# Performance work log

Hardware: AMD Instinct MI355X
Metric: run time of the kernel (lower is better)

## Reference

```python
import jax, jax.numpy as jnp
import numpy as np

MODES = 12

def _conv3x3_circular(x, w, b):
    # x: [B,C,H,W], w: [O,I,3,3] -> circular padding of 1 then VALID conv
    xp = jnp.pad(x, ((0, 0), (0, 0), (1, 1), (1, 1)), mode='wrap')
    y = jax.lax.conv_general_dilated(xp, w, window_strides=(1, 1), padding='VALID',
                                     dimension_numbers=('NCHW', 'OIHW', 'NCHW'))
    return y + b[None, :, None, None]

def _spectral_conv(x, w1, w2):
    # x: [B,C,H,W] real; w1, w2: [C,O,m1,m2] complex
    B, C, H, W = x.shape
    x_ft = jnp.fft.rfft2(x)  # [B,C,H,W//2+1] complex
    m1 = min(MODES, H // 2)
    m2 = min(MODES, W // 2 + 1)
    top = jnp.einsum('bixy,ioxy->boxy', x_ft[:, :, :m1, :m2], w1[:, :, :m1, :m2])
    bot = jnp.einsum('bixy,ioxy->boxy', x_ft[:, :, -m1:, :m2], w2[:, :, :m1, :m2])
    out_ft = jnp.zeros((B, w1.shape[1], H, W // 2 + 1), dtype=x_ft.dtype)
    out_ft = out_ft.at[:, :, :m1, :m2].set(top).at[:, :, -m1:, :m2].set(bot)
    return jnp.fft.irfft2(out_ft, s=(H, W))

def setup_inputs() -> dict:
    key = jax.random.key(0)
    ks = jax.random.split(key, 16)
    width = 32
    scale = 1.0 / (width * width)
    return {
        'x': jax.random.normal(ks[0], (64, 2, 128, 128), dtype=jnp.float32),
        'p_w': jax.random.normal(ks[1], (width, 2, 3, 3), dtype=jnp.float32) * 0.2,
        'p_b': jax.random.normal(ks[2], (width,), dtype=jnp.float32) * 0.1,
        'scw1r': jax.random.uniform(ks[3], (4, width, width, MODES, MODES), dtype=jnp.float32) * scale,
        'scw1i': jax.random.uniform(ks[4], (4, width, width, MODES, MODES), dtype=jnp.float32) * scale,
        'scw2r': jax.random.uniform(ks[5], (4, width, width, MODES, MODES), dtype=jnp.float32) * scale,
        'scw2i': jax.random.uniform(ks[6], (4, width, width, MODES, MODES), dtype=jnp.float32) * scale,
        'ww': jax.random.normal(ks[7], (4, width, width), dtype=jnp.float32) * (1.0 / np.sqrt(width)),
        'wb': jax.random.normal(ks[8], (4, width), dtype=jnp.float32) * 0.1,
        'q1_w': jax.random.normal(ks[9], (128, width), dtype=jnp.float32) * (1.0 / np.sqrt(width)),
        'q1_b': jax.random.normal(ks[10], (128,), dtype=jnp.float32) * 0.1,
        'q2_w': jax.random.normal(ks[11], (1, 128), dtype=jnp.float32) * (1.0 / np.sqrt(128.0)),
        'q2_b': jax.random.normal(ks[12], (1,), dtype=jnp.float32) * 0.1,
    }

def reference(x, p_w, p_b, scw1r, scw1i, scw2r, scw2i, ww, wb, q1_w, q1_b, q2_w, q2_b):
    h = _conv3x3_circular(x, p_w, p_b)  # lifting: [B,2,H,W] -> [B,width,H,W]
    for i in range(4):
        w1 = scw1r[i] + 1j * scw1i[i]
        w2 = scw2r[i] + 1j * scw2i[i]
        x1 = _spectral_conv(h, w1, w2)
        x2 = jnp.einsum('bihw,oi->bohw', h, ww[i]) + wb[i][None, :, None, None]
        h = jax.nn.gelu(x1 + x2, approximate=False)
    g = h.mean(axis=(2, 3))  # [B,width]
    g = jax.nn.gelu(g @ q1_w.T + q1_b, approximate=False)
    g = g @ q2_w.T + q2_b
    return jax.nn.sigmoid(g)
```

## Files before the change

### kernel.cpp

```cpp
#include <hip/hip_runtime.h>
#include <math.h>

#define B 64
#define CIN 2
#define CH 32
#define H 128
#define W 128
#define MODES 12
#define KY 24
#define KX 12
#define HW (H*W)
#define NMODE (KY*KX)

typedef float f32x2 __attribute__((ext_vector_type(2)));
__device__ __forceinline__ f32x2 mk2(float a, float b) { f32x2 r; r.x = a; r.y = b; return r; }

__device__ __forceinline__ float gelu_f(float x) {
    float ax = fabsf(x) * 0.70710678118654752f;
    float t  = __builtin_amdgcn_rcpf(1.0f + 0.3275911f * ax);
    float p  = t * (0.254829592f + t * (-0.284496736f + t * (1.421413741f +
               t * (-1.453152027f + t * 1.061405429f))));
    float e  = __expf(-ax * ax);
    float er = copysignf(1.0f - p * e, x);
    return 0.5f * x * (1.0f + er);
}

__global__ __launch_bounds__(256) void k_init_tables(
        float* cWkw, float* sWkw, float* cnsWwk,
        float* cnsH2, float* mnsH2) {
    int t = blockIdx.x * 256 + threadIdx.x;
    const float TWO_PI_OVER = 6.283185307179586476925f / 128.0f;
    if (t < MODES * W) {
        int k = t / W, w = t % W;
        int m = (k * w) & 127;
        float s, c;
        sincosf(TWO_PI_OVER * (float)m, &s, &c);
        cWkw[k * W + w] = c;  sWkw[k * W + w] = s;
        cnsWwk[(w * MODES + k) * 2]     = c;
        cnsWwk[(w * MODES + k) * 2 + 1] = -s;
    } else if (t < MODES * W + KY * H) {
        int u = t - MODES * W;
        int kyI = u / H, hh = u % H;
        int ky = (kyI < MODES) ? kyI : (H - MODES + (kyI - MODES));
        int m = (ky * hh) & 127;
        float s, c;
        sincosf(TWO_PI_OVER * (float)m, &s, &c);
        cnsH2[(hh * KY + kyI) * 2]     = c;
        cnsH2[(hh * KY + kyI) * 2 + 1] = s;
        mnsH2[(hh * KY + kyI) * 2]     = -s;
        mnsH2[(hh * KY + kyI) * 2 + 1] = c;
    }
}

__global__ __launch_bounds__(256) void k_reorder_w(
        const float* __restrict__ w1r, const float* __restrict__ w1i,
        const float* __restrict__ w2r, const float* __restrict__ w2i,
        float* __restrict__ wR) {
    int idx = blockIdx.x * 256 + threadIdx.x;
    if (idx >= 4 * NMODE * CH * CH) return;
    int o = idx & 31;
    int i = (idx >> 5) & 31;
    int m = (idx >> 10) % NMODE;
    int layer = idx / (NMODE * CH * CH);
    int kyI = m / KX, kx = m % KX;
    const float *sr, *si;
    int row;
    if (kyI < MODES) { sr = w1r; si = w1i; row = kyI; }
    else             { sr = w2r; si = w2i; row = kyI - MODES; }
    int src = ((layer * CH + i) * CH + o) * (MODES * MODES) + row * MODES + kx;
    wR[(size_t)idx * 2]     = sr[src];
    wR[(size_t)idx * 2 + 1] = si[src];
}

__global__ __launch_bounds__(256) void k_transpose_ww(
        const float* __restrict__ ww, float* __restrict__ wwT) {
    int idx = blockIdx.x * 256 + threadIdx.x;
    if (idx >= 4 * CH * CH) return;
    int l = idx / (CH * CH);
    int r = idx % (CH * CH);
    int i = r / CH, o = r % CH;
    wwT[idx] = ww[l * CH * CH + o * CH + i];
}

__global__ __launch_bounds__(128) void k_lift(
        const float* __restrict__ x, const float* __restrict__ pw,
        const float* __restrict__ pb, float* __restrict__ h) {
    int bh = blockIdx.x;
    int b = bh >> 7, hr = bh & 127;
    int w = threadIdx.x;
    int wl = (w + W - 1) & (W - 1), wr2 = (w + 1) & (W - 1);
    float xv[CIN][3][3];
    #pragma unroll
    for (int ic = 0; ic < CIN; ++ic) {
        const float* xc = x + (size_t)(b * CIN + ic) * HW;
        #pragma unroll
        for (int r = 0; r < 3; ++r) {
            int hh = (hr + r - 1 + H) & (H - 1);
            const float* xr = xc + hh * W;
            xv[ic][r][0] = xr[wl];
            xv[ic][r][1] = xr[w];
            xv[ic][r][2] = xr[wr2];
        }
    }
    for (int o = 0; o < CH; ++o) {
        float acc = pb[o];
        const float* wo = pw + o * CIN * 9;
        #pragma unroll
        for (int ic = 0; ic < CIN; ++ic)
            #pragma unroll
            for (int r = 0; r < 3; ++r)
                #pragma unroll
                for (int c3 = 0; c3 < 3; ++c3)
                    acc += xv[ic][r][c3] * wo[ic * 9 + r * 3 + c3];
        h[(size_t)(b * CH + o) * HW + hr * W + w] = acc;
    }
}

__global__ __launch_bounds__(256, 4) void k_dft_w(
        const float* __restrict__ h, const float* __restrict__ cnsWwk,
        float* __restrict__ Xw) {
    int row = blockIdx.x * 256 + threadIdx.x;
    const float* src = h + (size_t)row * W;
    f32x2 acc2[MODES];
    #pragma unroll
    for (int k = 0; k < MODES; ++k) acc2[k] = mk2(0.f, 0.f);
    for (int w4 = 0; w4 < W; w4 += 4) {
        float4 v = *(const float4*)(src + w4);
        #pragma unroll
        for (int j = 0; j < 4; ++j) {
            float xval = (j == 0) ? v.x : (j == 1) ? v.y : (j == 2) ? v.z : v.w;
            const f32x2* cns = (const f32x2*)(cnsWwk + (w4 + j) * MODES * 2);
            f32x2 xv2 = mk2(xval, xval);
            #pragma unroll
            for (int k = 0; k < MODES; ++k)
                acc2[k] += xv2 * cns[k];
        }
    }
    float2* dst = (float2*)(Xw + (size_t)row * MODES * 2);
    #pragma unroll
    for (int k = 0; k < MODES; ++k) dst[k] = make_float2(acc2[k].x, acc2[k].y);
}

__global__ __launch_bounds__(320) void k_dft_h(
        const float* __restrict__ Xw, const float* __restrict__ cnsH2,
        float* __restrict__ Xf) {
    __shared__ float4 xs4[H * KX / 2];
    const float2* xs = (const float2*)xs4;
    int bc = blockIdx.x;
    int tid = threadIdx.x;
    const float4* src = (const float4*)(Xw + (size_t)bc * H * KX * 2);
    #pragma unroll
    for (int r = 0; r < 3; ++r) {
        int idx = r * 320 + tid;
        if (idx < H * KX / 2) xs4[idx] = src[idx];
    }
    __syncthreads();
    if (tid < KY * KX) {
        int ky = tid / KX, kx = tid % KX;
        const float2* cs = (const float2*)cnsH2 + ky;
        float ar = 0.f, ai = 0.f;
        #pragma unroll 4
        for (int hh = 0; hh < H; ++hh) {
            float2 v = xs[hh * KX + kx];
            float2 t = cs[hh * KY];
            ar += v.x * t.x + v.y * t.y;
            ai += v.y * t.x - v.x * t.y;
        }
        ((float2*)Xf)[(size_t)tid * (B * CH) + bc] = make_float2(ar, ai);
    }
}

__global__ __launch_bounds__(256) void k_specmul(
        const float* __restrict__ Xf, const float* __restrict__ wRl,
        float* __restrict__ Yt) {
    int m = blockIdx.x;
    int o = threadIdx.x & 31;
    int bq = threadIdx.x >> 5;
    const f32x2* X  = (const f32x2*)Xf  + (size_t)m * (B * CH);
    const f32x2* Wm = (const f32x2*)wRl + (size_t)m * (CH * CH);
    f32x2 acc2[8];
    #pragma unroll
    for (int j = 0; j < 8; ++j) acc2[j] = mk2(0.f, 0.f);
    for (int i = 0; i < CH; ++i) {
        f32x2 wv  = Wm[i * CH + o];
        f32x2 wvB = mk2(-wv.y, wv.x);
        #pragma unroll
        for (int j = 0; j < 8; ++j) {
            f32x2 xv = X[(bq * 8 + j) * CH + i];
            acc2[j] += mk2(xv.x, xv.x) * wv + mk2(xv.y, xv.y) * wvB;
        }
    }
    float2* Yp = (float2*)Yt;
    #pragma unroll
    for (int j = 0; j < 8; ++j)
        Yp[((size_t)(bq * 8 + j) * NMODE + m) * CH + o] = make_float2(acc2[j].x, acc2[j].y);
}

__global__ __launch_bounds__(384) void k_idft_h(
        const float* __restrict__ Yt, const float* __restrict__ cnsH2,
        const float* __restrict__ mnsH2, float* __restrict__ Zt) {
    int b = blockIdx.x;
    int hh0 = blockIdx.y * 16;
    int o = threadIdx.x & 31;
    int kx = threadIdx.x >> 5;
    float yr[KY], yi[KY];
    #pragma unroll
    for (int ky = 0; ky < KY; ++ky) {
        float2 v = ((const float2*)Yt)[((size_t)b * NMODE + ky * KX + kx) * CH + o];
        yr[ky] = v.x;  yi[ky] = v.y;
    }
    float sc = (kx == 0 ? 1.0f : 2.0f) / (float)HW;
    #pragma unroll 2
    for (int hr = 0; hr < 16; ++hr) {
        int hh = hh0 + hr;
        const f32x2* cs = (const f32x2*)(cnsH2 + hh * KY * 2);
        const f32x2* ms = (const f32x2*)(mnsH2 + hh * KY * 2);
        f32x2 a = mk2(0.f, 0.f);
        #pragma unroll
        for (int ky = 0; ky < KY; ++ky)
            a += mk2(yr[ky], yr[ky]) * cs[ky] + mk2(yi[ky], yi[ky]) * ms[ky];
        size_t base = ((size_t)(b * H + hh) * 2) * (KX * CH) + kx * CH + o;
        Zt[base]            = a.x * sc;
        Zt[base + KX * CH]  = a.y * sc;
    }
}

template <int LAST>
__global__ __launch_bounds__(512, 4) void k_fused(
        float* __restrict__ h, const float* __restrict__ Zt,
        const float* __restrict__ wwT, const float* __restrict__ wb,
        const float* __restrict__ cWkw, const float* __restrict__ sWkw,
        float* __restrict__ part) {
    __shared__ float hs[CH * W];
    __shared__ float red[8][8];
    int bh = blockIdx.x;
    int b = bh >> 7, hr = bh & 127;
    int tid = threadIdx.x;
    int w = tid & 127;
    int og = __builtin_amdgcn_readfirstlane(tid >> 7);
    const float* hrow = h + (size_t)b * CH * HW + hr * W;
    #pragma unroll
    for (int r = 0; r < 2; ++r) {
        int f4 = r * 512 + tid;
        int i = f4 >> 5;
        int col = (f4 & 31) * 4;
        float4 v = *(const float4*)(hrow + (size_t)i * HW + col);
        *(float4*)(hs + i * W + col) = v;
    }
    float ck[MODES], nsk[MODES];
    #pragma unroll
    for (int k = 0; k < MODES; ++k) {
        ck[k]  = cWkw[k * W + w];
        nsk[k] = -sWkw[k * W + w];
    }
    float acc[8];
    const float* wbo = wb + og * 8;
    #pragma unroll
    for (int j = 0; j < 8; ++j) acc[j] = wbo[j];
    __syncthreads();
    #pragma unroll 4
    for (int i = 0; i < CH; ++i) {
        float hv = hs[i * W + w];
        const float* wt = wwT + i * CH + og * 8;
        #pragma unroll
        for (int j = 0; j < 8; ++j) acc[j] += hv * wt[j];
    }
    const float* Zb = Zt + ((size_t)bh * 2) * (KX * CH) + og * 8;
    #pragma unroll
    for (int k = 0; k < MODES; ++k) {
        const float* zr = Zb + k * CH;
        const float* zi = zr + KX * CH;
        float ckv = ck[k], nskv = nsk[k];
        #pragma unroll
        for (int j = 0; j < 8; ++j)
            acc[j] += zr[j] * ckv + zi[j] * nskv;
    }
    if (LAST == 0) {
        float* hout = h + (size_t)(b * CH + og * 8) * HW + hr * W + w;
        #pragma unroll
        for (int j = 0; j < 8; ++j)
            hout[(size_t)j * HW] = gelu_f(acc[j]);
    } else {
        float v[8];
        #pragma unroll
        for (int j = 0; j < 8; ++j) v[j] = gelu_f(acc[j]);
        #pragma unroll
        for (int j = 0; j < 8; ++j)
            #pragma unroll
            for (int off = 32; off > 0; off >>= 1)
                v[j] += __shfl_xor(v[j], off, 64);
        int wave = tid >> 6;
        if ((tid & 63) == 0) {
            #pragma unroll
            for (int j = 0; j < 8; ++j) red[wave][j] = v[j];
        }
        __syncthreads();
        if (tid < CH) {
            float p = red[2 * (tid >> 3)][tid & 7] + red[2 * (tid >> 3) + 1][tid & 7];
            part[((size_t)b * CH + tid) * H + hr] = p;
        }
    }
}

__global__ __launch_bounds__(64) void k_reduce(
        const float* __restrict__ part, float* __restrict__ g) {
    int bc = blockIdx.x;
    int t = threadIdx.x;
    float s = part[(size_t)bc * H + t] + part[(size_t)bc * H + 64 + t];
    #pragma unroll
    for (int off = 32; off > 0; off >>= 1) s += __shfl_down(s, off, 64);
    if (t == 0) g[bc] = s * (1.0f / (float)HW);
}

__global__ __launch_bounds__(128) void k_head(
        const float* __restrict__ g, const float* __restrict__ q1w,
        const float* __restrict__ q1b, const float* __restrict__ q2w,
        const float* __restrict__ q2b, float* __restrict__ out) {
    __shared__ float gs[CH];
    __shared__ float red2[2];
    int b = blockIdx.x;
    int t = threadIdx.x;
    if (t < CH) gs[t] = g[b * CH + t];
    __syncthreads();
    float a = q1b[t];
    #pragma unroll
    for (int c = 0; c < CH; ++c) a += gs[c] * q1w[t * CH + c];
    a = gelu_f(a);
    float hsum = a * q2w[t];
    #pragma unroll
    for (int off = 32; off > 0; off >>= 1) hsum += __shfl_down(hsum, off, 64);
    if ((t & 63) == 0) red2[t >> 6] = hsum;
    __syncthreads();
    if (t == 0) {
        float logit = red2[0] + red2[1] + q2b[0];
        out[b] = 1.0f / (1.0f + expf(-logit));
    }
}

extern "C" void kernel_launch(void* const* d_in, const int* in_sizes, int n_in,
                              void* d_out, int out_size, void* d_ws, size_t ws_size,
                              hipStream_t stream) {
    const float* x   = (const float*)d_in[0];
    const float* p_w = (const float*)d_in[1];
    const float* p_b = (const float*)d_in[2];
    const float* w1r = (const float*)d_in[3];
    const float* w1i = (const float*)d_in[4];
    const float* w2r = (const float*)d_in[5];
    const float* w2i = (const float*)d_in[6];
    const float* ww  = (const float*)d_in[7];
    const float* wb  = (const float*)d_in[8];
    const float* q1w = (const float*)d_in[9];
    const float* q1b = (const float*)d_in[10];
    const float* q2w = (const float*)d_in[11];
    const float* q2b = (const float*)d_in[12];
    float* out = (float*)d_out;

    float* ws = (float*)d_ws;
    size_t off = 0;
    auto alloc = [&](size_t n) {
        float* p = ws + off;
        off += (n + 63) & ~(size_t)63;
        return p;
    };
    float* cWkw   = alloc(MODES * W);
    float* sWkw   = alloc(MODES * W);
    float* cnsWwk = alloc(W * MODES * 2);
    float* cnsH2  = alloc(H * KY * 2);
    float* mnsH2  = alloc(H * KY * 2);
    float* hBuf = alloc((size_t)B * CH * HW);
    float* XwZ  = alloc((size_t)B * CH * H * KX * 2);
    float* Xf   = alloc((size_t)NMODE * B * CH * 2);
    float* Yt   = alloc((size_t)B * NMODE * CH * 2);
    float* wR   = alloc((size_t)4 * NMODE * CH * CH * 2);
    float* wwT  = alloc(4 * CH * CH);
    float* part = alloc((size_t)B * CH * H);
    float* g    = alloc(B * CH);

    k_init_tables<<<(MODES * W + KY * H + 255) / 256, 256, 0, stream>>>(
        cWkw, sWkw, cnsWwk, cnsH2, mnsH2);
    k_reorder_w<<<(4 * NMODE * CH * CH + 255) / 256, 256, 0, stream>>>(
        w1r, w1i, w2r, w2i, wR);
    k_transpose_ww<<<(4 * CH * CH + 255) / 256, 256, 0, stream>>>(ww, wwT);

    k_lift<<<B * H, 128, 0, stream>>>(x, p_w, p_b, hBuf);

    for (int layer = 0; layer < 4; ++layer) {
        k_dft_w<<<(B * CH * H) / 256, 256, 0, stream>>>(hBuf, cnsWwk, XwZ);
        k_dft_h<<<B * CH, 320, 0, stream>>>(XwZ, cnsH2, Xf);
        k_specmul<<<NMODE, 256, 0, stream>>>(
            Xf, wR + (size_t)layer * NMODE * CH * CH * 2, Yt);
        k_idft_h<<<dim3(B, 8), 384, 0, stream>>>(Yt, cnsH2, mnsH2, XwZ);
        if (layer < 3)
            k_fused<0><<<B * H, 512, 0, stream>>>(
                hBuf, XwZ, wwT + layer * CH * CH, wb + layer * CH, cWkw, sWkw, part);
        else
            k_fused<1><<<B * H, 512, 0, stream>>>(
                hBuf, XwZ, wwT + layer * CH * CH, wb + layer * CH, cWkw, sWkw, part);
    }

    k_reduce<<<B * CH, 64, 0, stream>>>(part, g);
    k_head<<<B, 128, 0, stream>>>(g, q1w, q1b, q2w, q2b, out);
}
```

Before: 888.4 us.

## Split row-wise W-DFT across four lanes with shuffle reduction and unified twiddle table

The W-direction DFT kernel now gives each row to four threads. Each thread loads 32 contiguous elements and computes partial sums for all 12 modes, then the four lanes combine results with xor shuffles and each writes 3 modes. This raises thread count and memory parallelism and shortens per-thread serial loops, at the cost of more shuffles and redundant twiddle loads. The cos/sin tables are merged into one interleaved k-major table shared by the DFT and fused kernels, replacing the separate cWkw/sWkw/cnsWwk arrays.

Result: slower. 2.079 ms (+134.1%).

```diff
diff --git a/kernel.cpp b/kernel.cpp
--- a/kernel.cpp
+++ b/kernel.cpp
@@ -26,8 +26,7 @@
 }
 
 __global__ __launch_bounds__(256) void k_init_tables(
-        float* cWkw, float* sWkw, float* cnsWwk,
-        float* cnsH2, float* mnsH2) {
+        float* cnsWkw, float* cnsH2, float* mnsH2) {
     int t = blockIdx.x * 256 + threadIdx.x;
     const float TWO_PI_OVER = 6.283185307179586476925f / 128.0f;
     if (t < MODES * W) {
@@ -35,9 +34,8 @@
         int m = (k * w) & 127;
         float s, c;
         sincosf(TWO_PI_OVER * (float)m, &s, &c);
-        cWkw[k * W + w] = c;  sWkw[k * W + w] = s;
-        cnsWwk[(w * MODES + k) * 2]     = c;
-        cnsWwk[(w * MODES + k) * 2 + 1] = -s;
+        cnsWkw[(k * W + w) * 2]     = c;
+        cnsWkw[(k * W + w) * 2 + 1] = -s;
     } else if (t < MODES * W + KY * H) {
         int u = t - MODES * W;
         int kyI = u / H, hh = u % H;
@@ -117,28 +115,42 @@
 }
 
 __global__ __launch_bounds__(256, 4) void k_dft_w(
-        const float* __restrict__ h, const float* __restrict__ cnsWwk,
+        const float* __restrict__ h, const float* __restrict__ cnsWkw,
         float* __restrict__ Xw) {
-    int row = blockIdx.x * 256 + threadIdx.x;
-    const float* src = h + (size_t)row * W;
-    f32x2 acc2[MODES];
-    #pragma unroll
-    for (int k = 0; k < MODES; ++k) acc2[k] = mk2(0.f, 0.f);
-    for (int w4 = 0; w4 < W; w4 += 4) {
-        float4 v = *(const float4*)(src + w4);
-        #pragma unroll
-        for (int j = 0; j < 4; ++j) {
-            float xval = (j == 0) ? v.x : (j == 1) ? v.y : (j == 2) ? v.z : v.w;
-            const f32x2* cns = (const f32x2*)(cnsWwk + (w4 + j) * MODES * 2);
-            f32x2 xv2 = mk2(xval, xval);
-            #pragma unroll
-            for (int k = 0; k < MODES; ++k)
-                acc2[k] += xv2 * cns[k];
-        }
+    int gt = blockIdx.x * 256 + threadIdx.x;
+    int row = gt >> 2, q = gt & 3;
+    const float4* src = (const float4*)(h + (size_t)row * W + q * 32);
+    float x[32];
+    #pragma unroll
+    for (int i = 0; i < 8; ++i) {
+        float4 v = src[i];
+        x[4 * i]     = v.x;  x[4 * i + 1] = v.y;
+        x[4 * i + 2] = v.z;  x[4 * i + 3] = v.w;
+    }
+    const f32x2* tw = (const f32x2*)cnsWkw + q * 32;
+    f32x2 acc[MODES];
+    #pragma unroll
+    for (int k = 0; k < MODES; ++k) {
+        f32x2 a = mk2(0.f, 0.f);
+        const f32x2* twk = tw + k * W;
+        #pragma unroll
+        for (int i = 0; i < 32; ++i)
+            a += mk2(x[i], x[i]) * twk[i];
+        acc[k] = a;
+    }
+    #pragma unroll
+    for (int k = 0; k < MODES; ++k) {
+        acc[k].x += __shfl_xor(acc[k].x, 1, 64);
+        acc[k].y += __shfl_xor(acc[k].y, 1, 64);
+        acc[k].x += __shfl_xor(acc[k].x, 2, 64);
+        acc[k].y += __shfl_xor(acc[k].y, 2, 64);
     }
     float2* dst = (float2*)(Xw + (size_t)row * MODES * 2);
     #pragma unroll
-    for (int k = 0; k < MODES; ++k) dst[k] = make_float2(acc2[k].x, acc2[k].y);
+    for (int j = 0; j < 3; ++j) {
+        int k = 3 * q + j;
+        dst[k] = make_float2(acc[k].x, acc[k].y);
+    }
 }
 
 __global__ __launch_bounds__(320) void k_dft_h(
@@ -229,7 +241,7 @@
 __global__ __launch_bounds__(512, 4) void k_fused(
         float* __restrict__ h, const float* __restrict__ Zt,
         const float* __restrict__ wwT, const float* __restrict__ wb,
-        const float* __restrict__ cWkw, const float* __restrict__ sWkw,
+        const float* __restrict__ cnsWkw,
         float* __restrict__ part) {
     __shared__ float hs[CH * W];
     __shared__ float red[8][8];
@@ -248,10 +260,12 @@
         *(float4*)(hs + i * W + col) = v;
     }
     float ck[MODES], nsk[MODES];
+    const f32x2* cns = (const f32x2*)cnsWkw;
     #pragma unroll
     for (int k = 0; k < MODES; ++k) {
-        ck[k]  = cWkw[k * W + w];
-        nsk[k] = -sWkw[k * W + w];
+        f32x2 p = cns[k * W + w];
+        ck[k]  = p.x;
+        nsk[k] = p.y;
     }
     float acc[8];
     const float* wbo = wb + og * 8;
@@ -362,9 +376,7 @@
         off += (n + 63) & ~(size_t)63;
         return p;
     };
-    float* cWkw   = alloc(MODES * W);
-    float* sWkw   = alloc(MODES * W);
-    float* cnsWwk = alloc(W * MODES * 2);
+    float* cnsWkw = alloc(MODES * W * 2);
     float* cnsH2  = alloc(H * KY * 2);
     float* mnsH2  = alloc(H * KY * 2);
     float* hBuf = alloc((size_t)B * CH * HW);
@@ -377,7 +389,7 @@
     float* g    = alloc(B * CH);
 
     k_init_tables<<<(MODES * W + KY * H + 255) / 256, 256, 0, stream>>>(
-        cWkw, sWkw, cnsWwk, cnsH2, mnsH2);
+        cnsWkw, cnsH2, mnsH2);
     k_reorder_w<<<(4 * NMODE * CH * CH + 255) / 256, 256, 0, stream>>>(
         w1r, w1i, w2r, w2i, wR);
     k_transpose_ww<<<(4 * CH * CH + 255) / 256, 256, 0, stream>>>(ww, wwT);
@@ -385,17 +397,17 @@
     k_lift<<<B * H, 128, 0, stream>>>(x, p_w, p_b, hBuf);
 
     for (int layer = 0; layer < 4; ++layer) {
-        k_dft_w<<<(B * CH * H) / 256, 256, 0, stream>>>(hBuf, cnsWwk, XwZ);
+        k_dft_w<<<(B * CH * H * 4) / 256, 256, 0, stream>>>(hBuf, cnsWkw, XwZ);
         k_dft_h<<<B * CH, 320, 0, stream>>>(XwZ, cnsH2, Xf);
         k_specmul<<<NMODE, 256, 0, stream>>>(
             Xf, wR + (size_t)layer * NMODE * CH * CH * 2, Yt);
         k_idft_h<<<dim3(B, 8), 384, 0, stream>>>(Yt, cnsH2, mnsH2, XwZ);
         if (layer < 3)
             k_fused<0><<<B * H, 512, 0, stream>>>(
-                hBuf, XwZ, wwT + layer * CH * CH, wb + layer * CH, cWkw, sWkw, part);
+                hBuf, XwZ, wwT + layer * CH * CH, wb + layer * CH, cnsWkw, part);
         else
             k_fused<1><<<B * H, 512, 0, stream>>>(
-                hBuf, XwZ, wwT + layer * CH * CH, wb + layer * CH, cWkw, sWkw, part);
+                hBuf, XwZ, wwT + layer * CH * CH, wb + layer * CH, cnsWkw, part);
     }
 
     k_reduce<<<B * CH, 64, 0, stream>>>(part, g);
```
